# Kernel optimization log

Measured on AMD Instinct MI355X. Metric: run time of the kernel, lower is better.

Reference implementation:

```python
import jax, jax.numpy as jnp
import numpy as np
import math

B, S, HID = 1, 2048, 1024
H = 16
D = HID // H          # head_dim = 64
M = 128               # RFF num_features
SIGMA = 1.0
ALPHA = 0.9
NORMALIZE = True


def setup_inputs() -> dict:
    key = jax.random.key(0)
    ks = jax.random.split(key, 12)
    s = 1.0 / math.sqrt(HID)  # nn.Linear default-ish init scale
    inp = {
        "hidden_states": jax.random.normal(ks[0], (B, S, HID), dtype=jnp.float32),
        "attention_mask": jnp.zeros((B, 1, 1, S), dtype=jnp.float32),  # 0 = attend
        "Wq": jax.random.uniform(ks[1], (HID, HID), minval=-s, maxval=s, dtype=jnp.float32),
        "bq": jnp.zeros((HID,), dtype=jnp.float32),
        "Wk": jax.random.uniform(ks[2], (HID, HID), minval=-s, maxval=s, dtype=jnp.float32),
        "bk": jnp.zeros((HID,), dtype=jnp.float32),
        "Wv": jax.random.uniform(ks[3], (HID, HID), minval=-s, maxval=s, dtype=jnp.float32),
        "bv": jnp.zeros((HID,), dtype=jnp.float32),
        "Wo": jax.random.uniform(ks[4], (HID, HID), minval=-s, maxval=s, dtype=jnp.float32),
        "bo": jnp.zeros((HID,), dtype=jnp.float32),
        # RFF kernel params per head: omega ~ N(0, 1/sigma^2), phase b ~ U[0, 2pi]
        "omega": jax.random.normal(ks[5], (H, D, M), dtype=jnp.float32) / SIGMA,
        "rff_b": jax.random.uniform(ks[6], (H, M), minval=0.0, maxval=2.0 * math.pi, dtype=jnp.float32),
    }
    return inp


def _heads(x):
    # (B, S, HID) -> (B, H, S, D)
    return x.reshape(B, S, H, D).transpose(0, 2, 1, 3)


def _phi(x, omega, rff_b):
    # x: (B, H, S, D) -> (B, H, S, M) random Fourier features
    proj = jnp.einsum("bhsd,hdm->bhsm", x, omega) + rff_b[None, :, None, :]
    phi = math.sqrt(2.0 / M) * jnp.cos(proj)
    if NORMALIZE:
        phi = phi / (jnp.linalg.norm(phi, axis=-1, keepdims=True) + 1e-6)
    return phi


def reference(hidden_states, attention_mask, Wq, bq, Wk, bk, Wv, bv, Wo, bo, omega, rff_b):
    q = _heads(hidden_states @ Wq.T + bq)   # (B,H,S,D)
    k = _heads(hidden_states @ Wk.T + bk)
    v = _heads(hidden_states @ Wv.T + bv)

    qn = q / (jnp.linalg.norm(q, axis=-1, keepdims=True) + 1e-6)
    kn = k / (jnp.linalg.norm(k, axis=-1, keepdims=True) + 1e-6)

    dot_scores = jnp.einsum("bhqd,bhkd->bhqk", q, k)             # standard QK^T
    kernel_scores = jnp.einsum("bhqm,bhkm->bhqk",
                               _phi(qn, omega, rff_b),
                               _phi(kn, omega, rff_b))            # phi(Q)phi(K)^T

    scores = (ALPHA * dot_scores + (1.0 - ALPHA) * kernel_scores) / math.sqrt(D)
    scores = scores + attention_mask * -10000.0
    weights = jax.nn.softmax(scores, axis=-1)                     # dropout: eval mode (identity)

    context = jnp.einsum("bhqk,bhkd->bhqd", weights, v)
    context = context.transpose(0, 2, 1, 3).reshape(B, S, HID)
    return context @ Wo.T + bo
```

## Files before the change

### kernel.cpp

```cpp
#include <hip/hip_runtime.h>
#include <math.h>

#define S_LEN 2048
#define HID   1024
#define NH    16
#define HD    64
#define NM    128
#define CAUG  192
#define KC2   32
#define NCH   32

constexpr float ALPHA = 0.9f;

typedef __attribute__((ext_vector_type(8))) short bf16x8;
typedef __attribute__((ext_vector_type(4))) short bf16x4;
typedef __attribute__((ext_vector_type(4))) float f32x4;
typedef __attribute__((ext_vector_type(4))) int   int4v;

#define MFMA(a,b,c) __builtin_amdgcn_mfma_f32_16x16x32_bf16(a,b,c,0,0,0)

static __device__ inline short f2bf(float f) {
    unsigned u = __float_as_uint(f);
    u += 0x7fffu + ((u >> 16) & 1u);
    return (short)(u >> 16);
}
static __device__ inline float bf2f(short s) {
    return __uint_as_float(((unsigned)(unsigned short)s) << 16);
}

__global__ __launch_bounds__(256)
void conv_kernel(const float* __restrict__ hs,
                 const float* __restrict__ Wq, const float* __restrict__ Wk,
                 const float* __restrict__ Wv, const float* __restrict__ Wo,
                 const float* __restrict__ omega,
                 short* __restrict__ hsb, short* __restrict__ wqb, short* __restrict__ wkb,
                 short* __restrict__ wvb, short* __restrict__ wob, short* __restrict__ omtb)
{
    int i = blockIdx.x * 256 + threadIdx.x;
    if (i >= 1605632) return;
    if (i >= 1572864) {
        int j = (i - 1572864) * 4;
        int h = j >> 13, rem = j & 8191;
        int d = rem >> 7, m = rem & 127;
        float4 v = *(const float4*)(omega + j);
        short* dst = omtb + ((h * 128 + m) << 6) + d;
        dst[0]       = f2bf(v.x);
        dst[64]      = f2bf(v.y);
        dst[128]     = f2bf(v.z);
        dst[192]     = f2bf(v.w);
        return;
    }
    const float* src; short* dst; int off;
    if (i < 524288) { src = hs; dst = hsb; off = i; }
    else {
        int j = i - 524288;
        int r = j >> 18;
        off = j & 262143;
        src = (r == 0) ? Wq : (r == 1) ? Wk : (r == 2) ? Wv : Wo;
        dst = (r == 0) ? wqb : (r == 1) ? wkb : (r == 2) ? wvb : wob;
    }
    float4 v = ((const float4*)src)[off];
    bf16x4 o; o[0] = f2bf(v.x); o[1] = f2bf(v.y); o[2] = f2bf(v.z); o[3] = f2bf(v.w);
    ((bf16x4*)dst)[off] = o;
}

__global__ __launch_bounds__(256)
void gemm_mfma(const short* __restrict__ A,
               const short* __restrict__ W0, const float* __restrict__ b0, void* C0,
               const short* __restrict__ W1, const float* __restrict__ b1, void* C1,
               const short* __restrict__ W2, const float* __restrict__ b2, void* C2,
               int m0_, int m1_, int m2_, int Mrows)
{
    const short* W; const float* bias; void* C; int mode;
    if (blockIdx.z == 0)      { W = W0; bias = b0; C = C0; mode = m0_; }
    else if (blockIdx.z == 1) { W = W1; bias = b1; C = C1; mode = m1_; }
    else                      { W = W2; bias = b2; C = C2; mode = m2_; }

    __shared__ short As[128][40];
    __shared__ short Bs[128][40];

    const int tid = threadIdx.x;
    const int wave = tid >> 6, lane = tid & 63;
    const int l15 = lane & 15, l4 = lane >> 4;
    const int wm = wave >> 1, wn = wave & 1;
    const int m0 = blockIdx.y * 128, n0 = blockIdx.x * 128;

    const int srow = (tid >> 2);
    const int scol = (tid & 3) * 16;

    f32x4 acc[4][4];
#pragma unroll
    for (int i = 0; i < 4; ++i)
#pragma unroll
        for (int j = 0; j < 4; ++j) acc[i][j] = (f32x4){0.f,0.f,0.f,0.f};

    int4v apre[2], bpre[2];
#pragma unroll
    for (int it = 0; it < 2; ++it) {
        apre[it] = *(const int4v*)((const char*)A + (size_t)(m0 + srow + it*64) * 2048 + scol);
        bpre[it] = *(const int4v*)((const char*)W + (size_t)(n0 + srow + it*64) * 2048 + scol);
    }

    for (int ks = 0; ks < 32; ++ks) {
        __syncthreads();
#pragma unroll
        for (int it = 0; it < 2; ++it) {
            *(int4v*)((char*)&As[0][0] + (srow + it*64) * 80 + scol) = apre[it];
            *(int4v*)((char*)&Bs[0][0] + (srow + it*64) * 80 + scol) = bpre[it];
        }
        __syncthreads();
        if (ks + 1 < 32) {
            const int kb = (ks + 1) * 64;
#pragma unroll
            for (int it = 0; it < 2; ++it) {
                apre[it] = *(const int4v*)((const char*)A + (size_t)(m0 + srow + it*64) * 2048 + kb + scol);
                bpre[it] = *(const int4v*)((const char*)W + (size_t)(n0 + srow + it*64) * 2048 + kb + scol);
            }
        }
        bf16x8 af[4], bf[4];
#pragma unroll
        for (int mi = 0; mi < 4; ++mi)
            af[mi] = *(const bf16x8*)((const char*)&As[0][0] + (wm*64 + mi*16 + l15) * 80 + l4*16);
#pragma unroll
        for (int nj = 0; nj < 4; ++nj)
            bf[nj] = *(const bf16x8*)((const char*)&Bs[0][0] + (wn*64 + nj*16 + l15) * 80 + l4*16);
#pragma unroll
        for (int mi = 0; mi < 4; ++mi)
#pragma unroll
            for (int nj = 0; nj < 4; ++nj)
                acc[mi][nj] = MFMA(af[mi], bf[nj], acc[mi][nj]);
    }

#pragma unroll
    for (int nj = 0; nj < 4; ++nj) {
        const int nglob = n0 + wn*64 + nj*16 + l15;
        const float bn = bias[nglob];
#pragma unroll
        for (int mi = 0; mi < 4; ++mi) {
            const int mbase = m0 + wm*64 + mi*16 + l4*4;
            if (mode == 0) {
#pragma unroll
                for (int r = 0; r < 4; ++r)
                    ((short*)C)[(size_t)(mbase + r) * 1024 + nglob] = f2bf(acc[mi][nj][r] + bn);
            } else if (mode == 1) {
                bf16x4 pk;
#pragma unroll
                for (int r = 0; r < 4; ++r) pk[r] = f2bf(acc[mi][nj][r] + bn);
                *(bf16x4*)((short*)C + (size_t)nglob * Mrows + mbase) = pk;
            } else {
#pragma unroll
                for (int r = 0; r < 4; ++r)
                    ((float*)C)[(size_t)(mbase + r) * 1024 + nglob] = acc[mi][nj][r] + bn;
            }
        }
    }
}

__global__ __launch_bounds__(256)
void phi2_kernel(const short* __restrict__ qbuf, const short* __restrict__ kbuf,
                 const short* __restrict__ omtb, const float* __restrict__ rffb,
                 short* __restrict__ Qa, short* __restrict__ Ka)
{
    __shared__ short om[128][72];
    __shared__ float bsh[128];

    const int src = blockIdx.z, h = blockIdx.y;
    const int s0 = blockIdx.x * 64;
    const short* X = src ? kbuf : qbuf;
    short* Out     = src ? Ka : Qa;
    const float fq   = src ? 1.0f : (ALPHA * 0.125f);
    const float fphi = src ? 1.0f : ((1.0f - ALPHA) * 0.125f);

    const int tid = threadIdx.x, wave = tid >> 6, lane = tid & 63;
    const int l15 = lane & 15, l4 = lane >> 4;

    {
        const char* gsrc = (const char*)(omtb + ((size_t)h << 13));
#pragma unroll
        for (int it = 0; it < 4; ++it) {
            int f = tid * 16 + it * 4096;
            int row = f >> 7, colb = f & 127;
            *(int4v*)((char*)&om[0][0] + row * 144 + colb) = *(const int4v*)(gsrc + f);
        }
        if (tid < 128) bsh[tid] = rffb[h * 128 + tid];
    }
    __syncthreads();

    const int srow = s0 + wave * 16 + l15;

    bf16x8 xf[2];
#pragma unroll
    for (int cs = 0; cs < 2; ++cs)
        xf[cs] = *(const bf16x8*)(X + (size_t)srow * HID + h * HD + cs * 32 + l4 * 8);

    float ss = 0.f;
#pragma unroll
    for (int cs = 0; cs < 2; ++cs)
#pragma unroll
        for (int j = 0; j < 8; ++j) { float v = bf2f(xf[cs][j]); ss = fmaf(v, v, ss); }
    ss += __shfl_xor(ss, 16);
    ss += __shfl_xor(ss, 32);
    const float inv = 1.0f / (sqrtf(ss) + 1e-6f);

    bf16x8 qn[2];
#pragma unroll
    for (int cs = 0; cs < 2; ++cs) {
        bf16x8 o, w;
#pragma unroll
        for (int j = 0; j < 8; ++j) {
            float v = bf2f(xf[cs][j]);
            o[j] = f2bf(v * inv);
            w[j] = f2bf(v * fq);
        }
        qn[cs] = o;
        *(bf16x8*)(Out + ((size_t)h * S_LEN + srow) * CAUG + cs * 32 + l4 * 8) = w;
    }

    f32x4 pacc[8];
#pragma unroll
    for (int t = 0; t < 8; ++t) pacc[t] = (f32x4){0.f,0.f,0.f,0.f};
#pragma unroll
    for (int t = 0; t < 8; ++t)
#pragma unroll
        for (int cs = 0; cs < 2; ++cs) {
            bf16x8 bf = *(const bf16x8*)((const char*)&om[0][0] + (t*16 + l15) * 144 + cs*64 + l4*16);
            pacc[t] = MFMA(qn[cs], bf, pacc[t]);
        }

    float ph[8][4];
    float ps[4] = {0.f, 0.f, 0.f, 0.f};
#pragma unroll
    for (int t = 0; t < 8; ++t) {
        const float bv = bsh[t * 16 + l15];
#pragma unroll
        for (int r = 0; r < 4; ++r) {
            float p = pacc[t][r] + bv;
            float c = 0.125f * __cosf(p);
            ph[t][r] = c;
            ps[r] = fmaf(c, c, ps[r]);
        }
    }
#pragma unroll
    for (int r = 0; r < 4; ++r) {
        ps[r] += __shfl_xor(ps[r], 1);
        ps[r] += __shfl_xor(ps[r], 2);
        ps[r] += __shfl_xor(ps[r], 4);
        ps[r] += __shfl_xor(ps[r], 8);
    }
    float inv2[4];
#pragma unroll
    for (int r = 0; r < 4; ++r) inv2[r] = fphi / (sqrtf(ps[r]) + 1e-6f);

#pragma unroll
    for (int t = 0; t < 8; ++t)
#pragma unroll
        for (int r = 0; r < 4; ++r)
            Out[((size_t)h * S_LEN + s0 + wave * 16 + l4 * 4 + r) * CAUG + 64 + t * 16 + l15]
                = f2bf(ph[t][r] * inv2[r]);
}

__global__ __launch_bounds__(256, 2)
void flash_mfma(const short* __restrict__ Qa, const short* __restrict__ Ka,
                const short* __restrict__ vt, const float* __restrict__ mask,
                short* __restrict__ ctxb)
{
    __shared__ short Ks[2][32][200];
    __shared__ short Vt[2][64][40];
    __shared__ short Pl[4][32][40];

    const int tid = threadIdx.x;
    const int wave = tid >> 6, lane = tid & 63;
    const int l15 = lane & 15, l4 = lane >> 4;
    const int g = wave >> 1, sub = wave & 1;
    const int h = blockIdx.y;
    const int q0 = blockIdx.x * 64 + sub * 32;

    bf16x8 qf[2][6];
#pragma unroll
    for (int qj = 0; qj < 2; ++qj)
#pragma unroll
        for (int cs = 0; cs < 6; ++cs)
            qf[qj][cs] = *(const bf16x8*)(Qa + ((size_t)h * 2048 + q0 + qj*16 + l15) * CAUG + cs*32 + l4*8);

    f32x4 oacc[4][2];
#pragma unroll
    for (int di = 0; di < 4; ++di)
#pragma unroll
        for (int qj = 0; qj < 2; ++qj) oacc[di][qj] = (f32x4){0.f,0.f,0.f,0.f};
    float lsum[2] = {0.f, 0.f};

    const int t = tid & 127;
    int kr[6], kcb[6], vr[2], vcb[2];
#pragma unroll
    for (int it = 0; it < 6; ++it) { int f = t*16 + it*2048; kr[it] = f/384; kcb[it] = f%384; }
#pragma unroll
    for (int it = 0; it < 2; ++it) { int f = t*16 + it*2048; vr[it] = f/64; vcb[it] = f%64; }

    const char* Kg = (const char*)(Ka + (size_t)h * 2048 * CAUG);
    const char* Vg = (const char*)(vt + (size_t)h * 64 * 2048);

    int4v kpre[6], vpre[2];
#pragma unroll
    for (int it = 0; it < 6; ++it)
        kpre[it] = *(const int4v*)(Kg + (size_t)(g*NCH)*12288 + (size_t)kr[it]*384 + kcb[it]);
#pragma unroll
    for (int it = 0; it < 2; ++it)
        vpre[it] = *(const int4v*)(Vg + (size_t)vr[it]*4096 + (size_t)(g*NCH)*64 + vcb[it]);

    for (int i = 0; i < NCH; ++i) {
        const int kt = g * NCH + i;
        __syncthreads();
#pragma unroll
        for (int it = 0; it < 6; ++it)
            *(int4v*)((char*)&Ks[g][0][0] + kr[it]*400 + kcb[it]) = kpre[it];
#pragma unroll
        for (int it = 0; it < 2; ++it)
            *(int4v*)((char*)&Vt[g][0][0] + vr[it]*80 + vcb[it]) = vpre[it];
        __syncthreads();
        if (i + 1 < NCH) {
            const size_t ko = (size_t)(kt + 1) * 12288;
            const size_t vo = (size_t)(kt + 1) * 64;
#pragma unroll
            for (int it = 0; it < 6; ++it)
                kpre[it] = *(const int4v*)(Kg + ko + (size_t)kr[it]*384 + kcb[it]);
#pragma unroll
            for (int it = 0; it < 2; ++it)
                vpre[it] = *(const int4v*)(Vg + (size_t)vr[it]*4096 + vo + vcb[it]);
        }

        f32x4 sacc[2][2];
#pragma unroll
        for (int fi = 0; fi < 2; ++fi)
#pragma unroll
            for (int qj = 0; qj < 2; ++qj) sacc[fi][qj] = (f32x4){0.f,0.f,0.f,0.f};
#pragma unroll
        for (int cs = 0; cs < 6; ++cs) {
            bf16x8 ka[2];
#pragma unroll
            for (int fi = 0; fi < 2; ++fi)
                ka[fi] = *(const bf16x8*)((const char*)&Ks[g][0][0] + (fi*16 + l15)*400 + cs*64 + l4*16);
#pragma unroll
            for (int fi = 0; fi < 2; ++fi)
#pragma unroll
                for (int qj = 0; qj < 2; ++qj)
                    sacc[fi][qj] = MFMA(ka[fi], qf[qj][cs], sacc[fi][qj]);
        }
#pragma unroll
        for (int fi = 0; fi < 2; ++fi) {
            float4 mk = *(const float4*)&mask[kt*32 + fi*16 + l4*4];
            float mv[4] = {mk.x * -10000.f, mk.y * -10000.f, mk.z * -10000.f, mk.w * -10000.f};
#pragma unroll
            for (int qj = 0; qj < 2; ++qj) {
                bf16x4 pk;
#pragma unroll
                for (int r = 0; r < 4; ++r) {
                    float p = __expf(sacc[fi][qj][r] + mv[r]);
                    lsum[qj] += p;
                    pk[r] = f2bf(p);
                }
                *(bf16x4*)((char*)&Pl[wave][0][0] + (qj*16 + l15)*80 + fi*32 + l4*8) = pk;
            }
        }
        {
            bf16x8 va[4], pb[2];
#pragma unroll
            for (int di = 0; di < 4; ++di)
                va[di] = *(const bf16x8*)((const char*)&Vt[g][0][0] + (di*16 + l15)*80 + l4*16);
#pragma unroll
            for (int qj = 0; qj < 2; ++qj)
                pb[qj] = *(const bf16x8*)((const char*)&Pl[wave][0][0] + (qj*16 + l15)*80 + l4*16);
#pragma unroll
            for (int di = 0; di < 4; ++di)
#pragma unroll
                for (int qj = 0; qj < 2; ++qj)
                    oacc[di][qj] = MFMA(va[di], pb[qj], oacc[di][qj]);
        }
    }

#pragma unroll
    for (int qj = 0; qj < 2; ++qj) {
        lsum[qj] += __shfl_xor(lsum[qj], 16);
        lsum[qj] += __shfl_xor(lsum[qj], 32);
    }

    __syncthreads();
    float* scrO = (float*)&Ks[0][0][0];
    float* scrL = (float*)&Vt[0][0][0];
    if (g == 1) {
#pragma unroll
        for (int qj = 0; qj < 2; ++qj) {
#pragma unroll
            for (int di = 0; di < 4; ++di)
                *(f32x4*)&scrO[(size_t)(sub*32 + qj*16 + l15)*68 + di*16 + l4*4] = oacc[di][qj];
            if (l4 == 0) scrL[sub*32 + qj*16 + l15] = lsum[qj];
        }
    }
    __syncthreads();
    if (g == 0) {
#pragma unroll
        for (int qj = 0; qj < 2; ++qj) {
            const float l = lsum[qj] + scrL[sub*32 + qj*16 + l15];
            const float inv = 1.0f / l;
            const int s = q0 + qj*16 + l15;
#pragma unroll
            for (int di = 0; di < 4; ++di) {
                f32x4 o2 = *(const f32x4*)&scrO[(size_t)(sub*32 + qj*16 + l15)*68 + di*16 + l4*4];
                bf16x4 ob;
#pragma unroll
                for (int r = 0; r < 4; ++r) ob[r] = f2bf((oacc[di][qj][r] + o2[r]) * inv);
                *(bf16x4*)(ctxb + (size_t)s * HID + h*64 + di*16 + l4*4) = ob;
            }
        }
    }
}

extern "C" void kernel_launch(void* const* d_in, const int* in_sizes, int n_in,
                              void* d_out, int out_size, void* d_ws, size_t ws_size,
                              hipStream_t stream)
{
    const float* hs    = (const float*)d_in[0];
    const float* mask  = (const float*)d_in[1];
    const float* Wq    = (const float*)d_in[2];
    const float* bq    = (const float*)d_in[3];
    const float* Wk    = (const float*)d_in[4];
    const float* bk    = (const float*)d_in[5];
    const float* Wv    = (const float*)d_in[6];
    const float* bv    = (const float*)d_in[7];
    const float* Wo    = (const float*)d_in[8];
    const float* bo    = (const float*)d_in[9];
    const float* omega = (const float*)d_in[10];
    const float* rffb  = (const float*)d_in[11];
    float* out = (float*)d_out;

    short* wsS = (short*)d_ws;
    short* hsb = wsS;
    short* wqb = hsb + 2097152;
    short* wkb = wqb + 1048576;
    short* wvb = wkb + 1048576;
    short* wob = wvb + 1048576;
    short* qb  = wob + 1048576;
    short* kb  = qb  + 2097152;
    short* vtb = kb  + 2097152;
    short* ctxb= vtb + 2097152;
    short* QaB = ctxb+ 2097152;
    short* KaB = QaB + 6291456;
    short* omtb= KaB + 6291456;

    conv_kernel<<<6272, 256, 0, stream>>>(hs, Wq, Wk, Wv, Wo, omega,
                                          hsb, wqb, wkb, wvb, wob, omtb);
    gemm_mfma<<<dim3(8, 16, 3), 256, 0, stream>>>(hsb, wqb, bq, qb, wkb, bk, kb, wvb, bv, vtb,
                                                  0, 0, 1, S_LEN);
    phi2_kernel<<<dim3(32, 16, 2), 256, 0, stream>>>(qb, kb, omtb, rffb, QaB, KaB);
    flash_mfma<<<dim3(32, 16), 256, 0, stream>>>(QaB, KaB, vtb, mask, ctxb);
    gemm_mfma<<<dim3(8, 16, 1), 256, 0, stream>>>(ctxb, wob, bo, out, wob, bo, out, wob, bo, out,
                                                  2, 2, 2, S_LEN);
}
```

Measured before the change: 127.6 us.

## Split flash attention keys across four waves with direct global K/V loads

Each block now handles 32 queries, and each of its four waves processes a separate quarter of the key sequence. K and V fragments are read directly from global memory, with no shared-memory staging and no block-wide barriers inside the loop. The four partial outputs and sums are combined through shared memory at the end. This raises the grid to twice as many blocks and allows 4 blocks per CU, removing sync overhead in exchange for uncoalesced, unreused global K/V reads that now rely on the cache.

```diff
diff --git a/kernel.cpp b/kernel.cpp
--- a/kernel.cpp
+++ b/kernel.cpp
@@ -7,8 +7,7 @@
 #define HD    64
 #define NM    128
 #define CAUG  192
-#define KC2   32
-#define NCH   32
+#define NCHW  16
 
 constexpr float ALPHA = 0.9f;
 
@@ -259,21 +258,20 @@
                 = f2bf(ph[t][r] * inv2[r]);
 }
 
-__global__ __launch_bounds__(256, 2)
+__global__ __launch_bounds__(256, 4)
 void flash_mfma(const short* __restrict__ Qa, const short* __restrict__ Ka,
                 const short* __restrict__ vt, const float* __restrict__ mask,
                 short* __restrict__ ctxb)
 {
-    __shared__ short Ks[2][32][200];
-    __shared__ short Vt[2][64][40];
-    __shared__ short Pl[4][32][40];
+    __shared__ char smem[26496];
 
     const int tid = threadIdx.x;
     const int wave = tid >> 6, lane = tid & 63;
     const int l15 = lane & 15, l4 = lane >> 4;
-    const int g = wave >> 1, sub = wave & 1;
     const int h = blockIdx.y;
-    const int q0 = blockIdx.x * 64 + sub * 32;
+    const int q0 = blockIdx.x * 32;
+
+    char* PlW = smem + wave * 2560;
 
     bf16x8 qf[2][6];
 #pragma unroll
@@ -289,44 +287,12 @@
         for (int qj = 0; qj < 2; ++qj) oacc[di][qj] = (f32x4){0.f,0.f,0.f,0.f};
     float lsum[2] = {0.f, 0.f};
 
-    const int t = tid & 127;
-    int kr[6], kcb[6], vr[2], vcb[2];
-#pragma unroll
-    for (int it = 0; it < 6; ++it) { int f = t*16 + it*2048; kr[it] = f/384; kcb[it] = f%384; }
-#pragma unroll
-    for (int it = 0; it < 2; ++it) { int f = t*16 + it*2048; vr[it] = f/64; vcb[it] = f%64; }
-
     const char* Kg = (const char*)(Ka + (size_t)h * 2048 * CAUG);
     const char* Vg = (const char*)(vt + (size_t)h * 64 * 2048);
 
-    int4v kpre[6], vpre[2];
-#pragma unroll
-    for (int it = 0; it < 6; ++it)
-        kpre[it] = *(const int4v*)(Kg + (size_t)(g*NCH)*12288 + (size_t)kr[it]*384 + kcb[it]);
-#pragma unroll
-    for (int it = 0; it < 2; ++it)
-        vpre[it] = *(const int4v*)(Vg + (size_t)vr[it]*4096 + (size_t)(g*NCH)*64 + vcb[it]);
-
-    for (int i = 0; i < NCH; ++i) {
-        const int kt = g * NCH + i;
-        __syncthreads();
-#pragma unroll
-        for (int it = 0; it < 6; ++it)
-            *(int4v*)((char*)&Ks[g][0][0] + kr[it]*400 + kcb[it]) = kpre[it];
-#pragma unroll
-        for (int it = 0; it < 2; ++it)
-            *(int4v*)((char*)&Vt[g][0][0] + vr[it]*80 + vcb[it]) = vpre[it];
-        __syncthreads();
-        if (i + 1 < NCH) {
-            const size_t ko = (size_t)(kt + 1) * 12288;
-            const size_t vo = (size_t)(kt + 1) * 64;
-#pragma unroll
-            for (int it = 0; it < 6; ++it)
-                kpre[it] = *(const int4v*)(Kg + ko + (size_t)kr[it]*384 + kcb[it]);
-#pragma unroll
-            for (int it = 0; it < 2; ++it)
-                vpre[it] = *(const int4v*)(Vg + (size_t)vr[it]*4096 + vo + vcb[it]);
-        }
+    for (int i = 0; i < NCHW; ++i) {
+        const int kt = wave * NCHW + i;
+        const char* kbase = Kg + (size_t)kt * 32 * 384;
 
         f32x4 sacc[2][2];
 #pragma unroll
@@ -338,13 +304,14 @@
             bf16x8 ka[2];
 #pragma unroll
             for (int fi = 0; fi < 2; ++fi)
-                ka[fi] = *(const bf16x8*)((const char*)&Ks[g][0][0] + (fi*16 + l15)*400 + cs*64 + l4*16);
+                ka[fi] = *(const bf16x8*)(kbase + (fi*16 + l15)*384 + cs*64 + l4*16);
 #pragma unroll
             for (int fi = 0; fi < 2; ++fi)
 #pragma unroll
                 for (int qj = 0; qj < 2; ++qj)
                     sacc[fi][qj] = MFMA(ka[fi], qf[qj][cs], sacc[fi][qj]);
         }
+
 #pragma unroll
         for (int fi = 0; fi < 2; ++fi) {
             float4 mk = *(const float4*)&mask[kt*32 + fi*16 + l4*4];
@@ -358,17 +325,18 @@
                     lsum[qj] += p;
                     pk[r] = f2bf(p);
                 }
-                *(bf16x4*)((char*)&Pl[wave][0][0] + (qj*16 + l15)*80 + fi*32 + l4*8) = pk;
+                *(bf16x4*)(PlW + (qj*16 + l15)*80 + fi*32 + l4*8) = pk;
             }
         }
+
         {
             bf16x8 va[4], pb[2];
 #pragma unroll
             for (int di = 0; di < 4; ++di)
-                va[di] = *(const bf16x8*)((const char*)&Vt[g][0][0] + (di*16 + l15)*80 + l4*16);
+                va[di] = *(const bf16x8*)(Vg + (size_t)(di*16 + l15)*4096 + kt*64 + l4*16);
 #pragma unroll
             for (int qj = 0; qj < 2; ++qj)
-                pb[qj] = *(const bf16x8*)((const char*)&Pl[wave][0][0] + (qj*16 + l15)*80 + l4*16);
+                pb[qj] = *(const bf16x8*)(PlW + (qj*16 + l15)*80 + l4*16);
 #pragma unroll
             for (int di = 0; di < 4; ++di)
 #pragma unroll
@@ -384,30 +352,35 @@
     }
 
     __syncthreads();
-    float* scrO = (float*)&Ks[0][0][0];
-    float* scrL = (float*)&Vt[0][0][0];
-    if (g == 1) {
+    float* scrO = (float*)smem;
+    float* scrL = (float*)(smem + 26112);
+    if (wave > 0) {
 #pragma unroll
         for (int qj = 0; qj < 2; ++qj) {
 #pragma unroll
             for (int di = 0; di < 4; ++di)
-                *(f32x4*)&scrO[(size_t)(sub*32 + qj*16 + l15)*68 + di*16 + l4*4] = oacc[di][qj];
-            if (l4 == 0) scrL[sub*32 + qj*16 + l15] = lsum[qj];
+                *(f32x4*)&scrO[(size_t)((wave-1)*32 + qj*16 + l15)*68 + di*16 + l4*4] = oacc[di][qj];
+            if (l4 == 0) scrL[(wave-1)*32 + qj*16 + l15] = lsum[qj];
         }
     }
     __syncthreads();
-    if (g == 0) {
+    if (wave == 0) {
 #pragma unroll
         for (int qj = 0; qj < 2; ++qj) {
-            const float l = lsum[qj] + scrL[sub*32 + qj*16 + l15];
+            float l = lsum[qj];
+#pragma unroll
+            for (int k = 0; k < 3; ++k) l += scrL[k*32 + qj*16 + l15];
             const float inv = 1.0f / l;
             const int s = q0 + qj*16 + l15;
 #pragma unroll
             for (int di = 0; di < 4; ++di) {
-                f32x4 o2 = *(const f32x4*)&scrO[(size_t)(sub*32 + qj*16 + l15)*68 + di*16 + l4*4];
+                f32x4 o = oacc[di][qj];
+#pragma unroll
+                for (int k = 0; k < 3; ++k)
+                    o += *(const f32x4*)&scrO[(size_t)(k*32 + qj*16 + l15)*68 + di*16 + l4*4];
                 bf16x4 ob;
 #pragma unroll
-                for (int r = 0; r < 4; ++r) ob[r] = f2bf((oacc[di][qj][r] + o2[r]) * inv);
+                for (int r = 0; r < 4; ++r) ob[r] = f2bf(o[r] * inv);
                 *(bf16x4*)(ctxb + (size_t)s * HID + h*64 + di*16 + l4*4) = ob;
             }
         }
@@ -451,7 +424,7 @@
     gemm_mfma<<<dim3(8, 16, 3), 256, 0, stream>>>(hsb, wqb, bq, qb, wkb, bk, kb, wvb, bv, vtb,
                                                   0, 0, 1, S_LEN);
     phi2_kernel<<<dim3(32, 16, 2), 256, 0, stream>>>(qb, kb, omtb, rffb, QaB, KaB);
-    flash_mfma<<<dim3(32, 16), 256, 0, stream>>>(QaB, KaB, vtb, mask, ctxb);
+    flash_mfma<<<dim3(64, 16), 256, 0, stream>>>(QaB, KaB, vtb, mask, ctxb);
     gemm_mfma<<<dim3(8, 16, 1), 256, 0, stream>>>(ctxb, wob, bo, out, wob, bo, out, wob, bo, out,
                                                   2, 2, 2, S_LEN);
 }
```

Measured after the change: 195.9 us. 53.5% more time.

## Double-buffer K tiles in LDS and load V fragments directly from global

Applied to the files above, without the earlier changes.

The flash attention loop now ping-pongs between two LDS buffers for the augmented K tile, so the next chunk's global loads and LDS stores overlap the current chunk's MFMA work. This halves the barriers per chunk. V fragments are read straight from global memory into registers instead of being staged through LDS. LDS use grows to 60 KB per block, which at launch bounds of 2 blocks per CU may limit occupancy, and the direct V reads are less coalesced.

```diff
diff --git a/kernel.cpp b/kernel.cpp
--- a/kernel.cpp
+++ b/kernel.cpp
@@ -7,7 +7,6 @@
 #define HD    64
 #define NM    128
 #define CAUG  192
-#define KC2   32
 #define NCH   32
 
 constexpr float ALPHA = 0.9f;
@@ -264,9 +263,7 @@
                 const short* __restrict__ vt, const float* __restrict__ mask,
                 short* __restrict__ ctxb)
 {
-    __shared__ short Ks[2][32][200];
-    __shared__ short Vt[2][64][40];
-    __shared__ short Pl[4][32][40];
+    __shared__ char smem[61440];
 
     const int tid = threadIdx.x;
     const int wave = tid >> 6, lane = tid & 63;
@@ -275,6 +272,10 @@
     const int h = blockIdx.y;
     const int q0 = blockIdx.x * 64 + sub * 32;
 
+    char* PlW  = smem + wave * 2560;
+    char* bufA = smem + 10240 + g * 25600;
+    char* bufB = bufA + 12800;
+
     bf16x8 qf[2][6];
 #pragma unroll
     for (int qj = 0; qj < 2; ++qj)
@@ -290,44 +291,34 @@
     float lsum[2] = {0.f, 0.f};
 
     const int t = tid & 127;
-    int kr[6], kcb[6], vr[2], vcb[2];
+    int kr[6], kcb[6];
 #pragma unroll
     for (int it = 0; it < 6; ++it) { int f = t*16 + it*2048; kr[it] = f/384; kcb[it] = f%384; }
-#pragma unroll
-    for (int it = 0; it < 2; ++it) { int f = t*16 + it*2048; vr[it] = f/64; vcb[it] = f%64; }
 
     const char* Kg = (const char*)(Ka + (size_t)h * 2048 * CAUG);
     const char* Vg = (const char*)(vt + (size_t)h * 64 * 2048);
-
-    int4v kpre[6], vpre[2];
-#pragma unroll
-    for (int it = 0; it < 6; ++it)
-        kpre[it] = *(const int4v*)(Kg + (size_t)(g*NCH)*12288 + (size_t)kr[it]*384 + kcb[it]);
-#pragma unroll
-    for (int it = 0; it < 2; ++it)
-        vpre[it] = *(const int4v*)(Vg + (size_t)vr[it]*4096 + (size_t)(g*NCH)*64 + vcb[it]);
-
-    for (int i = 0; i < NCH; ++i) {
-        const int kt = g * NCH + i;
-        __syncthreads();
+    const int base = g * NCH;
+
+    int4v kpre[6];
+    bf16x8 vA[4], vB[4];
+
+    auto loadKpre = [&](int kt) {
+        const char* kb = Kg + (size_t)kt * 12288;
 #pragma unroll
         for (int it = 0; it < 6; ++it)
-            *(int4v*)((char*)&Ks[g][0][0] + kr[it]*400 + kcb[it]) = kpre[it];
-#pragma unroll
-        for (int it = 0; it < 2; ++it)
-            *(int4v*)((char*)&Vt[g][0][0] + vr[it]*80 + vcb[it]) = vpre[it];
-        __syncthreads();
-        if (i + 1 < NCH) {
-            const size_t ko = (size_t)(kt + 1) * 12288;
-            const size_t vo = (size_t)(kt + 1) * 64;
-#pragma unroll
-            for (int it = 0; it < 6; ++it)
-                kpre[it] = *(const int4v*)(Kg + ko + (size_t)kr[it]*384 + kcb[it]);
-#pragma unroll
-            for (int it = 0; it < 2; ++it)
-                vpre[it] = *(const int4v*)(Vg + (size_t)vr[it]*4096 + vo + vcb[it]);
-        }
-
+            kpre[it] = *(const int4v*)(kb + (size_t)kr[it]*384 + kcb[it]);
+    };
+    auto writeStage = [&](char* buf) {
+#pragma unroll
+        for (int it = 0; it < 6; ++it)
+            *(int4v*)(buf + kr[it]*400 + kcb[it]) = kpre[it];
+    };
+    auto loadV = [&](bf16x8 (&dst)[4], int kt) {
+#pragma unroll
+        for (int di = 0; di < 4; ++di)
+            dst[di] = *(const bf16x8*)(Vg + (size_t)(di*16 + l15)*4096 + kt*64 + l4*16);
+    };
+    auto computeChunk = [&](const char* buf, const bf16x8 (&vf)[4], int kt) {
         f32x4 sacc[2][2];
 #pragma unroll
         for (int fi = 0; fi < 2; ++fi)
@@ -338,7 +329,7 @@
             bf16x8 ka[2];
 #pragma unroll
             for (int fi = 0; fi < 2; ++fi)
-                ka[fi] = *(const bf16x8*)((const char*)&Ks[g][0][0] + (fi*16 + l15)*400 + cs*64 + l4*16);
+                ka[fi] = *(const bf16x8*)(buf + (fi*16 + l15)*400 + cs*64 + l4*16);
 #pragma unroll
             for (int fi = 0; fi < 2; ++fi)
 #pragma unroll
@@ -358,23 +349,38 @@
                     lsum[qj] += p;
                     pk[r] = f2bf(p);
                 }
-                *(bf16x4*)((char*)&Pl[wave][0][0] + (qj*16 + l15)*80 + fi*32 + l4*8) = pk;
+                *(bf16x4*)(PlW + (qj*16 + l15)*80 + fi*32 + l4*8) = pk;
             }
         }
-        {
-            bf16x8 va[4], pb[2];
-#pragma unroll
-            for (int di = 0; di < 4; ++di)
-                va[di] = *(const bf16x8*)((const char*)&Vt[g][0][0] + (di*16 + l15)*80 + l4*16);
+        bf16x8 pb[2];
+#pragma unroll
+        for (int qj = 0; qj < 2; ++qj)
+            pb[qj] = *(const bf16x8*)(PlW + (qj*16 + l15)*80 + l4*16);
+#pragma unroll
+        for (int di = 0; di < 4; ++di)
 #pragma unroll
             for (int qj = 0; qj < 2; ++qj)
-                pb[qj] = *(const bf16x8*)((const char*)&Pl[wave][0][0] + (qj*16 + l15)*80 + l4*16);
-#pragma unroll
-            for (int di = 0; di < 4; ++di)
-#pragma unroll
-                for (int qj = 0; qj < 2; ++qj)
-                    oacc[di][qj] = MFMA(va[di], pb[qj], oacc[di][qj]);
-        }
+                oacc[di][qj] = MFMA(vf[di], pb[qj], oacc[di][qj]);
+    };
+
+    loadKpre(base);
+    writeStage(bufA);
+    loadV(vA, base);
+    __syncthreads();
+
+    for (int i = 0; i < NCH; i += 2) {
+        loadKpre(base + i + 1);
+        loadV(vB, base + i + 1);
+        computeChunk(bufA, vA, base + i);
+        writeStage(bufB);
+        __syncthreads();
+        if (i + 2 < NCH) {
+            loadKpre(base + i + 2);
+            loadV(vA, base + i + 2);
+        }
+        computeChunk(bufB, vB, base + i + 1);
+        if (i + 2 < NCH) writeStage(bufA);
+        __syncthreads();
     }
 
 #pragma unroll
@@ -383,9 +389,8 @@
         lsum[qj] += __shfl_xor(lsum[qj], 32);
     }
 
-    __syncthreads();
-    float* scrO = (float*)&Ks[0][0][0];
-    float* scrL = (float*)&Vt[0][0][0];
+    float* scrO = (float*)(smem + 10240);
+    float* scrL = (float*)(smem + 36352);
     if (g == 1) {
 #pragma unroll
         for (int qj = 0; qj < 2; ++qj) {
```

After: 135.8 us. 1.06x slower.

## Software-pipeline flash attention softmax behind next QK MFMA and halve GEMM M-tile

Applied to the files above, without the earlier changes.

The flash kernel now double-buffers the V tile and defers the softmax and PV product of each chunk by one iteration, so the exp/PV work of the previous tile overlaps the QK^T MFMAs and global prefetch of the current one. Shared memory becomes one manually carved buffer. Separately, the GEMM block tile shrinks from 128x128 to 64x128 and the grid doubles in M, which gives more blocks for the small projections at the cost of less reuse per block. The pipelining keeps extra score registers live, which may raise register pressure at the two-blocks-per-SM launch bound.

```diff
diff --git a/kernel.cpp b/kernel.cpp
--- a/kernel.cpp
+++ b/kernel.cpp
@@ -7,7 +7,6 @@
 #define HD    64
 #define NM    128
 #define CAUG  192
-#define KC2   32
 #define NCH   32
 
 constexpr float ALPHA = 0.9f;
@@ -76,56 +75,50 @@
     else if (blockIdx.z == 1) { W = W1; bias = b1; C = C1; mode = m1_; }
     else                      { W = W2; bias = b2; C = C2; mode = m2_; }
 
-    __shared__ short As[128][40];
+    __shared__ short As[64][40];
     __shared__ short Bs[128][40];
 
     const int tid = threadIdx.x;
     const int wave = tid >> 6, lane = tid & 63;
     const int l15 = lane & 15, l4 = lane >> 4;
     const int wm = wave >> 1, wn = wave & 1;
-    const int m0 = blockIdx.y * 128, n0 = blockIdx.x * 128;
-
-    const int srow = (tid >> 2);
+    const int m0 = blockIdx.y * 64, n0 = blockIdx.x * 128;
+
+    const int srow = tid >> 2;
     const int scol = (tid & 3) * 16;
 
-    f32x4 acc[4][4];
-#pragma unroll
-    for (int i = 0; i < 4; ++i)
+    f32x4 acc[2][4];
+#pragma unroll
+    for (int i = 0; i < 2; ++i)
 #pragma unroll
         for (int j = 0; j < 4; ++j) acc[i][j] = (f32x4){0.f,0.f,0.f,0.f};
 
-    int4v apre[2], bpre[2];
-#pragma unroll
-    for (int it = 0; it < 2; ++it) {
-        apre[it] = *(const int4v*)((const char*)A + (size_t)(m0 + srow + it*64) * 2048 + scol);
-        bpre[it] = *(const int4v*)((const char*)W + (size_t)(n0 + srow + it*64) * 2048 + scol);
-    }
+    int4v apre, bpre0, bpre1;
+    apre  = *(const int4v*)((const char*)A + (size_t)(m0 + srow) * 2048 + scol);
+    bpre0 = *(const int4v*)((const char*)W + (size_t)(n0 + srow) * 2048 + scol);
+    bpre1 = *(const int4v*)((const char*)W + (size_t)(n0 + 64 + srow) * 2048 + scol);
 
     for (int ks = 0; ks < 32; ++ks) {
         __syncthreads();
-#pragma unroll
-        for (int it = 0; it < 2; ++it) {
-            *(int4v*)((char*)&As[0][0] + (srow + it*64) * 80 + scol) = apre[it];
-            *(int4v*)((char*)&Bs[0][0] + (srow + it*64) * 80 + scol) = bpre[it];
-        }
+        *(int4v*)((char*)&As[0][0] + srow * 80 + scol) = apre;
+        *(int4v*)((char*)&Bs[0][0] + srow * 80 + scol) = bpre0;
+        *(int4v*)((char*)&Bs[0][0] + (64 + srow) * 80 + scol) = bpre1;
         __syncthreads();
         if (ks + 1 < 32) {
             const int kb = (ks + 1) * 64;
-#pragma unroll
-            for (int it = 0; it < 2; ++it) {
-                apre[it] = *(const int4v*)((const char*)A + (size_t)(m0 + srow + it*64) * 2048 + kb + scol);
-                bpre[it] = *(const int4v*)((const char*)W + (size_t)(n0 + srow + it*64) * 2048 + kb + scol);
-            }
-        }
-        bf16x8 af[4], bf[4];
-#pragma unroll
-        for (int mi = 0; mi < 4; ++mi)
-            af[mi] = *(const bf16x8*)((const char*)&As[0][0] + (wm*64 + mi*16 + l15) * 80 + l4*16);
+            apre  = *(const int4v*)((const char*)A + (size_t)(m0 + srow) * 2048 + kb + scol);
+            bpre0 = *(const int4v*)((const char*)W + (size_t)(n0 + srow) * 2048 + kb + scol);
+            bpre1 = *(const int4v*)((const char*)W + (size_t)(n0 + 64 + srow) * 2048 + kb + scol);
+        }
+        bf16x8 af[2], bf[4];
+#pragma unroll
+        for (int mi = 0; mi < 2; ++mi)
+            af[mi] = *(const bf16x8*)((const char*)&As[0][0] + (wm*32 + mi*16 + l15) * 80 + l4*16);
 #pragma unroll
         for (int nj = 0; nj < 4; ++nj)
             bf[nj] = *(const bf16x8*)((const char*)&Bs[0][0] + (wn*64 + nj*16 + l15) * 80 + l4*16);
 #pragma unroll
-        for (int mi = 0; mi < 4; ++mi)
+        for (int mi = 0; mi < 2; ++mi)
 #pragma unroll
             for (int nj = 0; nj < 4; ++nj)
                 acc[mi][nj] = MFMA(af[mi], bf[nj], acc[mi][nj]);
@@ -136,8 +129,8 @@
         const int nglob = n0 + wn*64 + nj*16 + l15;
         const float bn = bias[nglob];
 #pragma unroll
-        for (int mi = 0; mi < 4; ++mi) {
-            const int mbase = m0 + wm*64 + mi*16 + l4*4;
+        for (int mi = 0; mi < 2; ++mi) {
+            const int mbase = m0 + wm*32 + mi*16 + l4*4;
             if (mode == 0) {
 #pragma unroll
                 for (int r = 0; r < 4; ++r)
@@ -264,9 +257,7 @@
                 const short* __restrict__ vt, const float* __restrict__ mask,
                 short* __restrict__ ctxb)
 {
-    __shared__ short Ks[2][32][200];
-    __shared__ short Vt[2][64][40];
-    __shared__ short Pl[4][32][40];
+    __shared__ char smem[56320];
 
     const int tid = threadIdx.x;
     const int wave = tid >> 6, lane = tid & 63;
@@ -275,6 +266,11 @@
     const int h = blockIdx.y;
     const int q0 = blockIdx.x * 64 + sub * 32;
 
+    char* PlW  = smem + wave * 2560;
+    char* Kbuf = smem + 10240 + g * 12800;
+    char* Vt0  = smem + 35840 + g * 10240;
+    char* Vt1  = Vt0 + 5120;
+
     bf16x8 qf[2][6];
 #pragma unroll
     for (int qj = 0; qj < 2; ++qj)
@@ -298,84 +294,98 @@
 
     const char* Kg = (const char*)(Ka + (size_t)h * 2048 * CAUG);
     const char* Vg = (const char*)(vt + (size_t)h * 64 * 2048);
+    const int base = g * NCH;
 
     int4v kpre[6], vpre[2];
-#pragma unroll
-    for (int it = 0; it < 6; ++it)
-        kpre[it] = *(const int4v*)(Kg + (size_t)(g*NCH)*12288 + (size_t)kr[it]*384 + kcb[it]);
-#pragma unroll
-    for (int it = 0; it < 2; ++it)
-        vpre[it] = *(const int4v*)(Vg + (size_t)vr[it]*4096 + (size_t)(g*NCH)*64 + vcb[it]);
-
-    for (int i = 0; i < NCH; ++i) {
-        const int kt = g * NCH + i;
-        __syncthreads();
+    auto loadPre = [&](int kt) {
+        const char* kb = Kg + (size_t)kt * 12288;
 #pragma unroll
         for (int it = 0; it < 6; ++it)
-            *(int4v*)((char*)&Ks[g][0][0] + kr[it]*400 + kcb[it]) = kpre[it];
+            kpre[it] = *(const int4v*)(kb + (size_t)kr[it]*384 + kcb[it]);
 #pragma unroll
         for (int it = 0; it < 2; ++it)
-            *(int4v*)((char*)&Vt[g][0][0] + vr[it]*80 + vcb[it]) = vpre[it];
-        __syncthreads();
-        if (i + 1 < NCH) {
-            const size_t ko = (size_t)(kt + 1) * 12288;
-            const size_t vo = (size_t)(kt + 1) * 64;
-#pragma unroll
-            for (int it = 0; it < 6; ++it)
-                kpre[it] = *(const int4v*)(Kg + ko + (size_t)kr[it]*384 + kcb[it]);
-#pragma unroll
-            for (int it = 0; it < 2; ++it)
-                vpre[it] = *(const int4v*)(Vg + (size_t)vr[it]*4096 + vo + vcb[it]);
-        }
-
-        f32x4 sacc[2][2];
-#pragma unroll
-        for (int fi = 0; fi < 2; ++fi)
-#pragma unroll
-            for (int qj = 0; qj < 2; ++qj) sacc[fi][qj] = (f32x4){0.f,0.f,0.f,0.f};
-#pragma unroll
-        for (int cs = 0; cs < 6; ++cs) {
-            bf16x8 ka[2];
-#pragma unroll
-            for (int fi = 0; fi < 2; ++fi)
-                ka[fi] = *(const bf16x8*)((const char*)&Ks[g][0][0] + (fi*16 + l15)*400 + cs*64 + l4*16);
-#pragma unroll
-            for (int fi = 0; fi < 2; ++fi)
-#pragma unroll
-                for (int qj = 0; qj < 2; ++qj)
-                    sacc[fi][qj] = MFMA(ka[fi], qf[qj][cs], sacc[fi][qj]);
-        }
+            vpre[it] = *(const int4v*)(Vg + (size_t)vr[it]*4096 + kt*64 + vcb[it]);
+    };
+
+    f32x4 sacc_p[2][2];
+    float4 mkp0, mkp1;
+
+    auto softmax_pv = [&](char* Vbuf) {
 #pragma unroll
         for (int fi = 0; fi < 2; ++fi) {
-            float4 mk = *(const float4*)&mask[kt*32 + fi*16 + l4*4];
+            const float4 mk = fi ? mkp1 : mkp0;
             float mv[4] = {mk.x * -10000.f, mk.y * -10000.f, mk.z * -10000.f, mk.w * -10000.f};
 #pragma unroll
             for (int qj = 0; qj < 2; ++qj) {
                 bf16x4 pk;
 #pragma unroll
                 for (int r = 0; r < 4; ++r) {
-                    float p = __expf(sacc[fi][qj][r] + mv[r]);
+                    float p = __expf(sacc_p[fi][qj][r] + mv[r]);
                     lsum[qj] += p;
                     pk[r] = f2bf(p);
                 }
-                *(bf16x4*)((char*)&Pl[wave][0][0] + (qj*16 + l15)*80 + fi*32 + l4*8) = pk;
+                *(bf16x4*)(PlW + (qj*16 + l15)*80 + fi*32 + l4*8) = pk;
             }
         }
-        {
-            bf16x8 va[4], pb[2];
-#pragma unroll
-            for (int di = 0; di < 4; ++di)
-                va[di] = *(const bf16x8*)((const char*)&Vt[g][0][0] + (di*16 + l15)*80 + l4*16);
+        bf16x8 va[4], pb[2];
+#pragma unroll
+        for (int di = 0; di < 4; ++di)
+            va[di] = *(const bf16x8*)(Vbuf + (di*16 + l15)*80 + l4*16);
+#pragma unroll
+        for (int qj = 0; qj < 2; ++qj)
+            pb[qj] = *(const bf16x8*)(PlW + (qj*16 + l15)*80 + l4*16);
+#pragma unroll
+        for (int di = 0; di < 4; ++di)
 #pragma unroll
             for (int qj = 0; qj < 2; ++qj)
-                pb[qj] = *(const bf16x8*)((const char*)&Pl[wave][0][0] + (qj*16 + l15)*80 + l4*16);
-#pragma unroll
-            for (int di = 0; di < 4; ++di)
+                oacc[di][qj] = MFMA(va[di], pb[qj], oacc[di][qj]);
+    };
+
+    loadPre(base);
+
+    for (int i = 0; i < NCH; ++i) {
+        const int kt = base + i;
+        char* Vcur = (i & 1) ? Vt1 : Vt0;
+        __syncthreads();
+#pragma unroll
+        for (int it = 0; it < 6; ++it)
+            *(int4v*)(Kbuf + kr[it]*400 + kcb[it]) = kpre[it];
+#pragma unroll
+        for (int it = 0; it < 2; ++it)
+            *(int4v*)(Vcur + vr[it]*80 + vcb[it]) = vpre[it];
+        __syncthreads();
+
+        f32x4 sc[2][2];
+#pragma unroll
+        for (int fi = 0; fi < 2; ++fi)
+#pragma unroll
+            for (int qj = 0; qj < 2; ++qj) sc[fi][qj] = (f32x4){0.f,0.f,0.f,0.f};
+#pragma unroll
+        for (int cs = 0; cs < 6; ++cs) {
+            bf16x8 ka[2];
+#pragma unroll
+            for (int fi = 0; fi < 2; ++fi)
+                ka[fi] = *(const bf16x8*)(Kbuf + (fi*16 + l15)*400 + cs*64 + l4*16);
+#pragma unroll
+            for (int fi = 0; fi < 2; ++fi)
 #pragma unroll
                 for (int qj = 0; qj < 2; ++qj)
-                    oacc[di][qj] = MFMA(va[di], pb[qj], oacc[di][qj]);
-        }
-    }
+                    sc[fi][qj] = MFMA(ka[fi], qf[qj][cs], sc[fi][qj]);
+        }
+        float4 mkc0 = *(const float4*)&mask[kt*32 + l4*4];
+        float4 mkc1 = *(const float4*)&mask[kt*32 + 16 + l4*4];
+
+        if (i + 1 < NCH) loadPre(kt + 1);
+
+        if (i > 0) softmax_pv((i & 1) ? Vt0 : Vt1);
+
+#pragma unroll
+        for (int fi = 0; fi < 2; ++fi)
+#pragma unroll
+            for (int qj = 0; qj < 2; ++qj) sacc_p[fi][qj] = sc[fi][qj];
+        mkp0 = mkc0; mkp1 = mkc1;
+    }
+    softmax_pv(Vt1);
 
 #pragma unroll
     for (int qj = 0; qj < 2; ++qj) {
@@ -384,8 +394,8 @@
     }
 
     __syncthreads();
-    float* scrO = (float*)&Ks[0][0][0];
-    float* scrL = (float*)&Vt[0][0][0];
+    float* scrO = (float*)(smem + 10240);
+    float* scrL = (float*)(smem + 27648);
     if (g == 1) {
 #pragma unroll
         for (int qj = 0; qj < 2; ++qj) {
@@ -448,10 +458,10 @@
 
     conv_kernel<<<6272, 256, 0, stream>>>(hs, Wq, Wk, Wv, Wo, omega,
                                           hsb, wqb, wkb, wvb, wob, omtb);
-    gemm_mfma<<<dim3(8, 16, 3), 256, 0, stream>>>(hsb, wqb, bq, qb, wkb, bk, kb, wvb, bv, vtb,
+    gemm_mfma<<<dim3(8, 32, 3), 256, 0, stream>>>(hsb, wqb, bq, qb, wkb, bk, kb, wvb, bv, vtb,
                                                   0, 0, 1, S_LEN);
     phi2_kernel<<<dim3(32, 16, 2), 256, 0, stream>>>(qb, kb, omtb, rffb, QaB, KaB);
     flash_mfma<<<dim3(32, 16), 256, 0, stream>>>(QaB, KaB, vtb, mask, ctxb);
-    gemm_mfma<<<dim3(8, 16, 1), 256, 0, stream>>>(ctxb, wob, bo, out, wob, bo, out, wob, bo, out,
+    gemm_mfma<<<dim3(8, 32, 1), 256, 0, stream>>>(ctxb, wob, bo, out, wob, bo, out, wob, bo, out,
                                                   2, 2, 2, S_LEN);
 }
```

Result: faster. 119.1 us (-6.7%).
